# Performance work log

Hardware: AMD Instinct MI355X
Metric: run time of the kernel (lower is better)

The kernel has to match this reference:

```python
import jax, jax.numpy as jnp
import numpy as np

# Fixed LeNet C3 connection table: input channel i feeds these 10 output channels.
CONN = [[0, 4, 5, 6, 9, 10, 11, 12, 14, 15],
        [0, 1, 5, 6, 7, 10, 11, 12, 13, 15],
        [0, 1, 2, 6, 7, 8, 11, 13, 14, 15],
        [1, 2, 3, 6, 7, 8, 9, 12, 14, 15],
        [2, 3, 4, 7, 8, 9, 10, 12, 13, 15],
        [3, 4, 5, 8, 9, 10, 11, 13, 14, 15]]
# Static scatter indices: (out_channel, in_channel) pairs, 60 total.
_ROWS = np.concatenate([np.asarray(l, np.int32) for l in CONN])  # out-channel ids
_COLS = np.repeat(np.arange(6, dtype=np.int32), 10)              # in-channel ids


def setup_inputs() -> dict:
    key = jax.random.key(0)
    k1, k2 = jax.random.split(key)
    x = jax.random.normal(k1, (64, 6, 256, 256), jnp.float32)
    # kaiming-uniform-ish scale for 6*5*5 fan-in
    weight = jax.random.normal(k2, (10, 6, 5, 5), jnp.float32) * 0.1
    bias = jnp.full((1, 16, 1, 1), 0.01, jnp.float32)
    return {"x": x, "weight": weight, "bias": bias}


def reference(x, weight, bias):
    # Fold the per-input-channel loop + scatter-add into one dense [16,6,5,5]
    # kernel with zeros where the connection table is absent. Each iteration i
    # of the original adds conv(x[:,i], weight[j,i]) to out channel CONN[i][j].
    w_flat = weight.transpose(1, 0, 2, 3).reshape(60, 5, 5)  # ordered (i, j)
    w_full = jnp.zeros((16, 6, 5, 5), weight.dtype).at[_ROWS, _COLS].set(w_flat)
    # Bias for channel c is added once per list containing c -> multiply by count.
    counts = jnp.zeros((16,), weight.dtype).at[_ROWS].add(1.0)
    out = jax.lax.conv_general_dilated(
        x, w_full, window_strides=(1, 1), padding='VALID',
        dimension_numbers=('NCHW', 'OIHW', 'NCHW'))
    return out + bias * counts.reshape(1, 16, 1, 1)
```

## Files before the change

kernel.cpp:

```cpp
#include <hip/hip_runtime.h>
#include <hip/hip_fp16.h>

typedef _Float16 f16x8 __attribute__((ext_vector_type(8)));
typedef float f32x4 __attribute__((ext_vector_type(4)));

__device__ constexpr int CONN[6][10] = {
    {0, 4, 5, 6, 9, 10, 11, 12, 14, 15},
    {0, 1, 5, 6, 7, 10, 11, 12, 13, 15},
    {0, 1, 2, 6, 7, 8, 11, 13, 14, 15},
    {1, 2, 3, 6, 7, 8, 9, 12, 14, 15},
    {2, 3, 4, 7, 8, 9, 10, 12, 13, 15},
    {3, 4, 5, 8, 9, 10, 11, 13, 14, 15}};

__device__ constexpr int CNT[16] = {3,3,3,3,3,3,4,4,4,4,4,4,4,4,4,6};

__device__ __forceinline__ f16x8 u4_to_h8(uint4 u) { f16x8 r; __builtin_memcpy(&r, &u, 16); return r; }

__global__ void prep_A(const float* __restrict__ w, unsigned short* __restrict__ Wp) {
    int t = blockIdx.x * 256 + threadIdx.x;
    if (t >= 5120) return;
    int j = t & 7, lane = (t >> 3) & 63, ks = t >> 9;
    int ch = lane & 15, kb = lane >> 4;
    float val = 0.f;
    if (kb < 3 && j < 5) {
        int ii = 2 * kb + (ks >= 5 ? 1 : 0);
        int r  = (ks >= 5) ? ks - 5 : ks;
        for (int jj = 0; jj < 10; ++jj)
            if (CONN[ii][jj] == ch) val = w[jj * 150 + ii * 25 + r * 5 + j];
    }
    __half h = __float2half(val);
    unsigned short u; __builtin_memcpy(&u, &h, 2);
    Wp[t] = u;
}

__global__ __launch_bounds__(256, 4) void c3_mfma(
    const float* __restrict__ x, const unsigned short* __restrict__ Wp,
    const float* __restrict__ bias, float* __restrict__ out)
{
    __shared__ char s_raw[6 * 35 * 152];

    const int tid = threadIdx.x;
    int bid = blockIdx.x;
    int id = (bid & 7) * 288 + (bid >> 3);
    const int bx = id & 3;
    const int by = (id >> 2) % 9;
    const int n  = id / 36;
    const int X0 = bx * 64;
    const int Y0 = by * 30;
    const float* xin = x + (size_t)n * 6 * 65536;

    for (int i = tid; i < 6 * 35 * 18; i += 256) {
        int c4  = i % 18;
        int t   = i / 18;
        int row = t % 35;
        int ch  = t / 35;
        int gr  = Y0 + row; if (gr > 255) gr = 255;
        int gc4 = (X0 >> 2) + c4; if (gc4 > 63) gc4 = 63;
        float4 v = *reinterpret_cast<const float4*>(xin + (size_t)ch * 65536 + gr * 256 + gc4 * 4);
        __half2 lo = __floats2half2_rn(v.x, v.y);
        __half2 hi = __floats2half2_rn(v.z, v.w);
        uint2 u; __builtin_memcpy(&u.x, &lo, 4); __builtin_memcpy(&u.y, &hi, 4);
        *reinterpret_cast<uint2*>(s_raw + (ch * 35 + row) * 152 + c4 * 8) = u;
    }
    __syncthreads();

    const unsigned* s_dw = reinterpret_cast<const unsigned*>(s_raw);
    const int lane = tid & 63;
    const int wv   = tid >> 6;
    const int nn   = lane & 15;
    const int kb   = lane >> 4;

    f16x8 W[10];
    const uint4* wp4 = reinterpret_cast<const uint4*>(Wp);
    #pragma unroll
    for (int ks = 0; ks < 10; ++ks) W[ks] = u4_to_h8(wp4[ks * 64 + lane]);

    const int iiA = (kb < 3) ? 2 * kb : 0;
    const int dwoff = (32 * wv + 2 * nn) >> 2;
    const unsigned shb = (unsigned)((nn & 1) * 16);

    auto loadf = [&](int dwaddr) -> f16x8 {
        unsigned e0 = s_dw[dwaddr],     e1 = s_dw[dwaddr + 1],
                 e2 = s_dw[dwaddr + 2], e3 = s_dw[dwaddr + 3],
                 e4 = s_dw[dwaddr + 4];
        unsigned o0 = (unsigned)((((unsigned long long)e1 << 32) | e0) >> shb);
        unsigned o1 = (unsigned)((((unsigned long long)e2 << 32) | e1) >> shb);
        unsigned o2 = (unsigned)((((unsigned long long)e3 << 32) | e2) >> shb);
        unsigned o3 = (unsigned)((((unsigned long long)e4 << 32) | e3) >> shb);
        return u4_to_h8(make_uint4(o0, o1, o2, o3));
    };

    const int r0dw = iiA * 35 * 38 + dwoff;
    f16x8 A0 = loadf(r0dw + 0 * 38), A1 = loadf(r0dw + 1 * 38),
          A2 = loadf(r0dw + 2 * 38), A3 = loadf(r0dw + 3 * 38),
          A4 = loadf(r0dw + 4 * 38);
    f16x8 B0 = loadf(r0dw + 1330 + 0 * 38), B1 = loadf(r0dw + 1330 + 1 * 38),
          B2 = loadf(r0dw + 1330 + 2 * 38), B3 = loadf(r0dw + 1330 + 3 * 38),
          B4 = loadf(r0dw + 1330 + 4 * 38);
    int aN = r0dw + 5 * 38;

    const int gx = X0 + wv * 16 + nn;
    const bool xok = gx < 252;
    float bb[4];
    #pragma unroll
    for (int q = 0; q < 4; ++q) {
        int ch = kb * 4 + q;
        bb[q] = bias[ch] * (float)CNT[ch];
    }
    float* const op0 = out + (size_t)n * 16 * 63504 + (size_t)(kb * 4) * 63504 + gx;
    int yoff = Y0 * 252;
    int gy = Y0;

#define PHASE(a0,a1,a2,a3,a4,b0,b1,b2,b3,b4)                                    \
    {                                                                           \
        f32x4 accA = {bb[0], bb[1], bb[2], bb[3]};                              \
        f32x4 accB = {0.f, 0.f, 0.f, 0.f};                                      \
        accA = __builtin_amdgcn_mfma_f32_16x16x32_f16(W[0], a0, accA, 0, 0, 0); \
        accB = __builtin_amdgcn_mfma_f32_16x16x32_f16(W[5], b0, accB, 0, 0, 0); \
        a0 = loadf(aN); b0 = loadf(aN + 1330); aN += 38;                        \
        accA = __builtin_amdgcn_mfma_f32_16x16x32_f16(W[1], a1, accA, 0, 0, 0); \
        accB = __builtin_amdgcn_mfma_f32_16x16x32_f16(W[6], b1, accB, 0, 0, 0); \
        accA = __builtin_amdgcn_mfma_f32_16x16x32_f16(W[2], a2, accA, 0, 0, 0); \
        accB = __builtin_amdgcn_mfma_f32_16x16x32_f16(W[7], b2, accB, 0, 0, 0); \
        accA = __builtin_amdgcn_mfma_f32_16x16x32_f16(W[3], a3, accA, 0, 0, 0); \
        accB = __builtin_amdgcn_mfma_f32_16x16x32_f16(W[8], b3, accB, 0, 0, 0); \
        accA = __builtin_amdgcn_mfma_f32_16x16x32_f16(W[4], a4, accA, 0, 0, 0); \
        accB = __builtin_amdgcn_mfma_f32_16x16x32_f16(W[9], b4, accB, 0, 0, 0); \
        if (gy < 252 && xok) {                                                  \
            f32x4 acc = accA + accB;                                            \
            op0[0 * 63504 + yoff] = acc[0];                                     \
            op0[1 * 63504 + yoff] = acc[1];                                     \
            op0[2 * 63504 + yoff] = acc[2];                                     \
            op0[3 * 63504 + yoff] = acc[3];                                     \
        }                                                                       \
        ++gy; yoff += 252;                                                      \
    }

    #pragma unroll 1
    for (int g = 0; g < 6; ++g) {
        PHASE(A0, A1, A2, A3, A4, B0, B1, B2, B3, B4)
        PHASE(A1, A2, A3, A4, A0, B1, B2, B3, B4, B0)
        PHASE(A2, A3, A4, A0, A1, B2, B3, B4, B0, B1)
        PHASE(A3, A4, A0, A1, A2, B3, B4, B0, B1, B2)
        PHASE(A4, A0, A1, A2, A3, B4, B0, B1, B2, B3)
    }
#undef PHASE
}

extern "C" void kernel_launch(void* const* d_in, const int* in_sizes, int n_in,
                              void* d_out, int out_size, void* d_ws, size_t ws_size,
                              hipStream_t stream) {
    const float* x    = (const float*)d_in[0];
    const float* w    = (const float*)d_in[1];
    const float* bias = (const float*)d_in[2];
    float* out = (float*)d_out;
    unsigned short* Wp = (unsigned short*)d_ws;

    hipLaunchKernelGGL(prep_A, dim3(20), dim3(256), 0, stream, w, Wp);
    hipLaunchKernelGGL(c3_mfma, dim3(2304), dim3(256), 0, stream, x, Wp, bias, out);
}
```

Measured before the change: 129.2 us.

## Retile C3 conv into full-width 12-row strips with inner column loop

Each block now stages a full-width 16-row strip of all six input planes (12 output rows) into LDS and loops over four 64-column tiles inside the block, instead of a 64x30 tile with column halos. This removes horizontal halo reloads and clamping, gives fully coalesced row loads, and drops the row bound check because 21 strips of 12 rows exactly cover 252 outputs. In exchange the vertical halo overhead rises (16 rows loaded per 12 produced), LDS per block grows, the occupancy hint drops from 4 to 3 blocks per CU, and the register window is reloaded per column tile.

```diff
diff --git a/kernel.cpp b/kernel.cpp
--- a/kernel.cpp
+++ b/kernel.cpp
@@ -16,6 +16,9 @@
 
 __device__ __forceinline__ f16x8 u4_to_h8(uint4 u) { f16x8 r; __builtin_memcpy(&r, &u, 16); return r; }
 
+#define PITCH_DW 132
+#define PLANE_DW (17 * 132)
+
 __global__ void prep_A(const float* __restrict__ w, unsigned short* __restrict__ Wp) {
     int t = blockIdx.x * 256 + threadIdx.x;
     if (t >= 5120) return;
@@ -33,38 +36,39 @@
     Wp[t] = u;
 }
 
-__global__ __launch_bounds__(256, 4) void c3_mfma(
+__global__ __launch_bounds__(256, 3) void c3_mfma(
     const float* __restrict__ x, const unsigned short* __restrict__ Wp,
     const float* __restrict__ bias, float* __restrict__ out)
 {
-    __shared__ char s_raw[6 * 35 * 152];
+    __shared__ unsigned s_lds[6 * PLANE_DW];
 
     const int tid = threadIdx.x;
-    int bid = blockIdx.x;
-    int id = (bid & 7) * 288 + (bid >> 3);
-    const int bx = id & 3;
-    const int by = (id >> 2) % 9;
-    const int n  = id / 36;
-    const int X0 = bx * 64;
-    const int Y0 = by * 30;
+    const int id = (blockIdx.x & 7) * 168 + (blockIdx.x >> 3);
+    const int by = id % 21;
+    const int n  = id / 21;
+    const int Y0 = by * 12;
     const float* xin = x + (size_t)n * 6 * 65536;
 
-    for (int i = tid; i < 6 * 35 * 18; i += 256) {
-        int c4  = i % 18;
-        int t   = i / 18;
-        int row = t % 35;
-        int ch  = t / 35;
-        int gr  = Y0 + row; if (gr > 255) gr = 255;
-        int gc4 = (X0 >> 2) + c4; if (gc4 > 63) gc4 = 63;
-        float4 v = *reinterpret_cast<const float4*>(xin + (size_t)ch * 65536 + gr * 256 + gc4 * 4);
+    #pragma unroll 4
+    for (int it = 0; it < 24; ++it) {
+        int i   = tid + it * 256;
+        int c4  = i & 63;
+        int row = (i >> 6) & 15;
+        int ch  = i >> 10;
+        float4 v = *reinterpret_cast<const float4*>(
+            xin + (size_t)ch * 65536 + (size_t)(Y0 + row) * 256 + c4 * 4);
         __half2 lo = __floats2half2_rn(v.x, v.y);
         __half2 hi = __floats2half2_rn(v.z, v.w);
         uint2 u; __builtin_memcpy(&u.x, &lo, 4); __builtin_memcpy(&u.y, &hi, 4);
-        *reinterpret_cast<uint2*>(s_raw + (ch * 35 + row) * 152 + c4 * 8) = u;
+        *reinterpret_cast<uint2*>(&s_lds[ch * PLANE_DW + row * PITCH_DW + c4 * 2]) = u;
+    }
+    if (tid < 96) {
+        int ch = tid >> 4, row = tid & 15;
+        *reinterpret_cast<uint2*>(&s_lds[ch * PLANE_DW + row * PITCH_DW + 128]) =
+            make_uint2(0u, 0u);
     }
     __syncthreads();
 
-    const unsigned* s_dw = reinterpret_cast<const unsigned*>(s_raw);
     const int lane = tid & 63;
     const int wv   = tid >> 6;
     const int nn   = lane & 15;
@@ -76,13 +80,12 @@
     for (int ks = 0; ks < 10; ++ks) W[ks] = u4_to_h8(wp4[ks * 64 + lane]);
 
     const int iiA = (kb < 3) ? 2 * kb : 0;
-    const int dwoff = (32 * wv + 2 * nn) >> 2;
     const unsigned shb = (unsigned)((nn & 1) * 16);
 
     auto loadf = [&](int dwaddr) -> f16x8 {
-        unsigned e0 = s_dw[dwaddr],     e1 = s_dw[dwaddr + 1],
-                 e2 = s_dw[dwaddr + 2], e3 = s_dw[dwaddr + 3],
-                 e4 = s_dw[dwaddr + 4];
+        unsigned e0 = s_lds[dwaddr],     e1 = s_lds[dwaddr + 1],
+                 e2 = s_lds[dwaddr + 2], e3 = s_lds[dwaddr + 3],
+                 e4 = s_lds[dwaddr + 4];
         unsigned o0 = (unsigned)((((unsigned long long)e1 << 32) | e0) >> shb);
         unsigned o1 = (unsigned)((((unsigned long long)e2 << 32) | e1) >> shb);
         unsigned o2 = (unsigned)((((unsigned long long)e3 << 32) | e2) >> shb);
@@ -90,26 +93,12 @@
         return u4_to_h8(make_uint4(o0, o1, o2, o3));
     };
 
-    const int r0dw = iiA * 35 * 38 + dwoff;
-    f16x8 A0 = loadf(r0dw + 0 * 38), A1 = loadf(r0dw + 1 * 38),
-          A2 = loadf(r0dw + 2 * 38), A3 = loadf(r0dw + 3 * 38),
-          A4 = loadf(r0dw + 4 * 38);
-    f16x8 B0 = loadf(r0dw + 1330 + 0 * 38), B1 = loadf(r0dw + 1330 + 1 * 38),
-          B2 = loadf(r0dw + 1330 + 2 * 38), B3 = loadf(r0dw + 1330 + 3 * 38),
-          B4 = loadf(r0dw + 1330 + 4 * 38);
-    int aN = r0dw + 5 * 38;
-
-    const int gx = X0 + wv * 16 + nn;
-    const bool xok = gx < 252;
     float bb[4];
     #pragma unroll
     for (int q = 0; q < 4; ++q) {
         int ch = kb * 4 + q;
         bb[q] = bias[ch] * (float)CNT[ch];
     }
-    float* const op0 = out + (size_t)n * 16 * 63504 + (size_t)(kb * 4) * 63504 + gx;
-    int yoff = Y0 * 252;
-    int gy = Y0;
 
 #define PHASE(a0,a1,a2,a3,a4,b0,b1,b2,b3,b4)                                    \
     {                                                                           \
@@ -117,7 +106,7 @@
         f32x4 accB = {0.f, 0.f, 0.f, 0.f};                                      \
         accA = __builtin_amdgcn_mfma_f32_16x16x32_f16(W[0], a0, accA, 0, 0, 0); \
         accB = __builtin_amdgcn_mfma_f32_16x16x32_f16(W[5], b0, accB, 0, 0, 0); \
-        a0 = loadf(aN); b0 = loadf(aN + 1330); aN += 38;                        \
+        a0 = loadf(aN); b0 = loadf(aN + 2244); aN += PITCH_DW;                  \
         accA = __builtin_amdgcn_mfma_f32_16x16x32_f16(W[1], a1, accA, 0, 0, 0); \
         accB = __builtin_amdgcn_mfma_f32_16x16x32_f16(W[6], b1, accB, 0, 0, 0); \
         accA = __builtin_amdgcn_mfma_f32_16x16x32_f16(W[2], a2, accA, 0, 0, 0); \
@@ -126,23 +115,44 @@
         accB = __builtin_amdgcn_mfma_f32_16x16x32_f16(W[8], b3, accB, 0, 0, 0); \
         accA = __builtin_amdgcn_mfma_f32_16x16x32_f16(W[4], a4, accA, 0, 0, 0); \
         accB = __builtin_amdgcn_mfma_f32_16x16x32_f16(W[9], b4, accB, 0, 0, 0); \
-        if (gy < 252 && xok) {                                                  \
+        if (xok) {                                                              \
             f32x4 acc = accA + accB;                                            \
             op0[0 * 63504 + yoff] = acc[0];                                     \
             op0[1 * 63504 + yoff] = acc[1];                                     \
             op0[2 * 63504 + yoff] = acc[2];                                     \
             op0[3 * 63504 + yoff] = acc[3];                                     \
         }                                                                       \
-        ++gy; yoff += 252;                                                      \
+        yoff += 252;                                                            \
     }
 
     #pragma unroll 1
-    for (int g = 0; g < 6; ++g) {
+    for (int t = 0; t < 4; ++t) {
+        const int gx = 64 * t + 16 * wv + nn;
+        const bool xok = gx < 252;
+        const int baseA = iiA * PLANE_DW + (gx >> 1);
+        f16x8 A0 = loadf(baseA + 0 * PITCH_DW), A1 = loadf(baseA + 1 * PITCH_DW),
+              A2 = loadf(baseA + 2 * PITCH_DW), A3 = loadf(baseA + 3 * PITCH_DW),
+              A4 = loadf(baseA + 4 * PITCH_DW);
+        f16x8 B0 = loadf(baseA + 2244 + 0 * PITCH_DW), B1 = loadf(baseA + 2244 + 1 * PITCH_DW),
+              B2 = loadf(baseA + 2244 + 2 * PITCH_DW), B3 = loadf(baseA + 2244 + 3 * PITCH_DW),
+              B4 = loadf(baseA + 2244 + 4 * PITCH_DW);
+        int aN = baseA + 5 * PITCH_DW;
+
+        float* const op0 = out + (size_t)n * 16 * 63504 + (size_t)(kb * 4) * 63504 + gx;
+        int yoff = Y0 * 252;
+
         PHASE(A0, A1, A2, A3, A4, B0, B1, B2, B3, B4)
         PHASE(A1, A2, A3, A4, A0, B1, B2, B3, B4, B0)
         PHASE(A2, A3, A4, A0, A1, B2, B3, B4, B0, B1)
         PHASE(A3, A4, A0, A1, A2, B3, B4, B0, B1, B2)
         PHASE(A4, A0, A1, A2, A3, B4, B0, B1, B2, B3)
+        PHASE(A0, A1, A2, A3, A4, B0, B1, B2, B3, B4)
+        PHASE(A1, A2, A3, A4, A0, B1, B2, B3, B4, B0)
+        PHASE(A2, A3, A4, A0, A1, B2, B3, B4, B0, B1)
+        PHASE(A3, A4, A0, A1, A2, B3, B4, B0, B1, B2)
+        PHASE(A4, A0, A1, A2, A3, B4, B0, B1, B2, B3)
+        PHASE(A0, A1, A2, A3, A4, B0, B1, B2, B3, B4)
+        PHASE(A1, A2, A3, A4, A0, B1, B2, B3, B4, B0)
     }
 #undef PHASE
 }
@@ -157,5 +167,5 @@
     unsigned short* Wp = (unsigned short*)d_ws;
 
     hipLaunchKernelGGL(prep_A, dim3(20), dim3(256), 0, stream, w, Wp);
-    hipLaunchKernelGGL(c3_mfma, dim3(2304), dim3(256), 0, stream, x, Wp, bias, out);
+    hipLaunchKernelGGL(c3_mfma, dim3(1344), dim3(256), 0, stream, x, Wp, bias, out);
 }
```

Result: faster. 110.3 us (-14.6%).
